# Optimization experiments

Measured on AMD Instinct MI355X. Metric: run time of the kernel, lower is better.

The kernel has to match this reference:

```python
import jax, jax.numpy as jnp
import numpy as np
from jax import lax

DN = ('NCH', 'OIH', 'NCH')

def conv1d(x, w, b, pad=0):
    y = lax.conv_general_dilated(x, w, window_strides=(1,), padding=[(pad, pad)], dimension_numbers=DN)
    return y + b[None, :, None]

def conv_transpose1d(x, w_torch, b):
    # torch ConvTranspose1d weight: [C_in, C_out, K]; equivalent to full conv with flipped kernel
    k = w_torch.shape[-1]
    w = jnp.flip(jnp.transpose(w_torch, (1, 0, 2)), axis=-1)  # [C_out, C_in, K]
    y = lax.conv_general_dilated(x, w, window_strides=(1,), padding=[(k - 1, k - 1)], dimension_numbers=DN)
    return y + b[None, :, None]

def converter(signal, w1, b1, w2, b2, wt, bt, w3, b3):
    h = jax.nn.relu(conv1d(signal, w1, b1))          # [B,10,n-2]
    h = jax.nn.relu(conv1d(h, w2, b2))               # [B,10,n-2]
    h = jax.nn.relu(conv_transpose1d(h, wt, bt))     # [B,10,n]
    h = jax.nn.sigmoid(conv1d(h, w3, b3))            # [B,2,n]
    return h

def setup_inputs() -> dict:
    key = jax.random.key(0)
    ks = jax.random.split(key, 12)
    B, C, n = 32, 128, 8192
    signal = jax.random.normal(ks[0], (B, C, n), dtype=jnp.float32)
    curr_diag = jax.random.uniform(ks[1], (B, n - 1), dtype=jnp.float32) + 0.5
    s = 0.1
    return {
        'signal': signal,
        'curr_diag': curr_diag,
        'index_diag': 1,
        'w1': jax.random.normal(ks[2], (10, C, 3), dtype=jnp.float32) * s,
        'b1': jax.random.normal(ks[3], (10,), dtype=jnp.float32) * s,
        'w2': jax.random.normal(ks[4], (10, 10, 1), dtype=jnp.float32) * s,
        'b2': jax.random.normal(ks[5], (10,), dtype=jnp.float32) * s,
        'wt': jax.random.normal(ks[6], (10, 10, 3), dtype=jnp.float32) * s,
        'bt': jax.random.normal(ks[7], (10,), dtype=jnp.float32) * s,
        'w3': jax.random.normal(ks[8], (2, 10, 1), dtype=jnp.float32) * s,
        'b3': jax.random.normal(ks[9], (2,), dtype=jnp.float32) * s,
        'const': jnp.float32(0.99),
    }

def reference(signal, curr_diag, index_diag, w1, b1, w2, b2, wt, bt, w3, b3, const):
    n = signal.shape[-1]
    lr = converter(signal, w1, b1, w2, b2, wt, bt, w3, b3)  # [B,2,n]
    left, right = lr[:, 0, :], lr[:, 1, :]
    # diag_len = n - index_diag; next diag has length diag_len - 1
    mass_in = curr_diag[:, 1:] * right[:, 1:n - index_diag]
    mass_in = mass_in + curr_diag[:, :-1] * left[:, index_diag:n - 1]
    mass_out = right[:, 0:n - index_diag - 1] + left[:, index_diag + 1:n]
    next_diag = const * mass_in / mass_out
    next_diag = jnp.log(next_diag)
    next_diag = next_diag - jnp.mean(next_diag)
    return next_diag
```

## Files before the change

kernel.cpp:

```cpp
#include <hip/hip_runtime.h>
#include <math.h>

#define B     32
#define CIN   128
#define NN    8192
#define N1    8190
#define CH    10
#define TOUT  252
#define NTILE 33

__global__ void k0_prep(const float* __restrict__ w1, float* __restrict__ wT)
{
    const int i = blockIdx.x * 256 + threadIdx.x;
    if (i < CIN * 32) {
        const int ci = i >> 5, r = i & 31;
        float v = 0.f;
        if (r < 30) {
            const int o = r / 3, k = r - o * 3;
            v = w1[(o * CIN + ci) * 3 + k];
        }
        wT[i] = v;
    }
}

__global__ __launch_bounds__(256, 4) void k_main(
    const float* __restrict__ sig, const float* __restrict__ wT,
    const float* __restrict__ b1, const float* __restrict__ w2, const float* __restrict__ b2,
    const float* __restrict__ wt, const float* __restrict__ bt,
    const float* __restrict__ w3, const float* __restrict__ b3,
    const float* __restrict__ cd, const float* __restrict__ cstp,
    float* __restrict__ outv, float* __restrict__ bsums)
{
    __shared__ float h2s[CH * 256];
    __shared__ float lsh[256], rsh[256];
    __shared__ float red[256];

    const int tid = threadIdx.x;
    const int b   = blockIdx.y;
    const int t0  = blockIdx.x * TOUT;
    const int g   = t0 - 2 + tid;
    const bool gvalid = (g >= 0) && (g < N1);
    const bool sh = (g > NN - 4);
    int gl = (g < 0) ? 0 : g;
    if (gl > NN - 4) gl = NN - 4;
    const float* sb = sig + (size_t)b * CIN * NN + gl;

    float y[CH];
#pragma unroll
    for (int o = 0; o < CH; ++o) y[o] = b1[o];

    for (int c = 0; c < 8; ++c) {
        float4 v[16];
#pragma unroll
        for (int j = 0; j < 16; ++j)
            v[j] = *(const float4*)(sb + (size_t)(c * 16 + j) * NN);

        const float* wbase = wT + c * 16 * 32;
#pragma unroll
        for (int j = 0; j < 16; ++j) {
            const float s0 = sh ? v[j].y : v[j].x;
            const float s1 = sh ? v[j].z : v[j].y;
            const float s2 = sh ? v[j].w : v[j].z;
            const float* wrow = wbase + j * 32;
#pragma unroll
            for (int o = 0; o < CH; ++o) {
                y[o] = fmaf(wrow[o * 3 + 0], s0, y[o]);
                y[o] = fmaf(wrow[o * 3 + 1], s1, y[o]);
                y[o] = fmaf(wrow[o * 3 + 2], s2, y[o]);
            }
        }
    }

#pragma unroll
    for (int o = 0; o < CH; ++o) y[o] = fmaxf(y[o], 0.f);
#pragma unroll
    for (int o = 0; o < CH; ++o) {
        float a = b2[o];
#pragma unroll
        for (int i = 0; i < CH; ++i) a = fmaf(w2[o * CH + i], y[i], a);
        h2s[o * 256 + tid] = gvalid ? fmaxf(a, 0.f) : 0.f;
    }
    __syncthreads();

    const int s = t0 + tid;
    if (tid < 254 && s < NN) {
        float acc[CH];
#pragma unroll
        for (int o = 0; o < CH; ++o) acc[o] = bt[o];
#pragma unroll
        for (int i = 0; i < CH; ++i) {
            const float a0 = h2s[i * 256 + tid];
            const float a1 = h2s[i * 256 + tid + 1];
            const float a2 = h2s[i * 256 + tid + 2];
            const float* wp = wt + i * CH * 3;
#pragma unroll
            for (int o = 0; o < CH; ++o) {
                acc[o] = fmaf(wp[o * 3 + 0], a2, acc[o]);
                acc[o] = fmaf(wp[o * 3 + 1], a1, acc[o]);
                acc[o] = fmaf(wp[o * 3 + 2], a0, acc[o]);
            }
        }
        float l = b3[0], r = b3[1];
#pragma unroll
        for (int o = 0; o < CH; ++o) {
            const float h3 = fmaxf(acc[o], 0.f);
            l = fmaf(w3[o],      h3, l);
            r = fmaf(w3[CH + o], h3, r);
        }
        lsh[tid] = 1.f / (1.f + __expf(-l));
        rsh[tid] = 1.f / (1.f + __expf(-r));
    }
    __syncthreads();

    float vlog = 0.f;
    const int t = t0 + tid;
    if (tid < TOUT && t < N1) {
        const float c0 = cd[(size_t)b * (NN - 1) + t];
        const float c1 = cd[(size_t)b * (NN - 1) + t + 1];
        const float mi = c1 * rsh[tid + 1] + c0 * lsh[tid + 1];
        const float mo = rsh[tid] + lsh[tid + 2];
        vlog = __logf(cstp[0] * mi / mo);
        outv[(size_t)b * N1 + t] = vlog;
    }

    red[tid] = vlog;
    __syncthreads();
#pragma unroll
    for (int st = 128; st > 0; st >>= 1) {
        if (tid < st) red[tid] += red[tid + st];
        __syncthreads();
    }
    if (tid == 0) bsums[blockIdx.y * NTILE + blockIdx.x] = red[0];
}

__global__ __launch_bounds__(256) void k3_meansub(
    const float* __restrict__ bsums, float* __restrict__ outv, int n)
{
    __shared__ float red[256];
    const int tid = threadIdx.x;
    float s = 0.f;
    for (int i = tid; i < NTILE * B; i += 256) s += bsums[i];
    red[tid] = s;
    __syncthreads();
#pragma unroll
    for (int st = 128; st > 0; st >>= 1) {
        if (tid < st) red[tid] += red[tid + st];
        __syncthreads();
    }
    const float mean = red[0] / (float)(B * N1);
    __syncthreads();
    const int i = blockIdx.x * 256 + tid;
    if (i < n) outv[i] -= mean;
}

extern "C" void kernel_launch(void* const* d_in, const int* in_sizes, int n_in,
                              void* d_out, int out_size, void* d_ws, size_t ws_size,
                              hipStream_t stream)
{
    const float* sig = (const float*)d_in[0];
    const float* cd  = (const float*)d_in[1];
    const float* w1  = (const float*)d_in[3];
    const float* b1  = (const float*)d_in[4];
    const float* w2  = (const float*)d_in[5];
    const float* b2  = (const float*)d_in[6];
    const float* wt  = (const float*)d_in[7];
    const float* bt  = (const float*)d_in[8];
    const float* w3  = (const float*)d_in[9];
    const float* b3  = (const float*)d_in[10];
    const float* cst = (const float*)d_in[11];

    float* outv = (float*)d_out;

    float* ws   = (float*)d_ws;
    float* wT   = ws;
    float* bsum = wT + CIN * 32;

    dim3 blk(256);

    k0_prep   <<<dim3(16), blk, 0, stream>>>(w1, wT);
    k_main    <<<dim3(NTILE, B), blk, 0, stream>>>(sig, wT, b1, w2, b2,
                                                   wt, bt, w3, b3, cd, cst, outv, bsum);
    k3_meansub<<<dim3((out_size + 255) / 256), blk, 0, stream>>>(bsum, outv, out_size);
}
```

Baseline: 243.8 us.

## Stage signal chunks into LDS via direct global-to-LDS loads

Replaces the per-thread float4 register loads of 16 channels with wave-cooperative global_load_lds transfers into a shared buffer. Each thread then reads its three-tap window from LDS. The output tile shrinks to 244 columns with 34 tiles, and the tile start is clamped so every load stays a full aligned 256-column row. The aim is fully coalesced aligned loads with lower register pressure. The cost is extra barriers per chunk, serialised load and compute with no double buffering, and more halo overlap between tiles.

```diff
diff --git a/kernel.cpp b/kernel.cpp
--- a/kernel.cpp
+++ b/kernel.cpp
@@ -1,13 +1,23 @@
 #include <hip/hip_runtime.h>
 #include <math.h>
 
-#define B     32
-#define CIN   128
-#define NN    8192
-#define N1    8190
-#define CH    10
-#define TOUT  252
-#define NTILE 33
+#define B      32
+#define CIN    128
+#define NN     8192
+#define N1     8190
+#define CH     10
+#define TOUT   244
+#define NTILE  34
+#define SCOLS  256
+#define CPC    16
+#define NCHUNK (CIN / CPC)
+
+__device__ __forceinline__ void load_lds16(const float* g, float* l)
+{
+    __builtin_amdgcn_global_load_lds(
+        (const __attribute__((address_space(1))) void*)g,
+        (__attribute__((address_space(3))) void*)l, 16, 0, 0);
+}
 
 __global__ void k0_prep(const float* __restrict__ w1, float* __restrict__ wT)
 {
@@ -31,46 +41,55 @@
     const float* __restrict__ cd, const float* __restrict__ cstp,
     float* __restrict__ outv, float* __restrict__ bsums)
 {
+    __shared__ float sigb[CPC * SCOLS];
     __shared__ float h2s[CH * 256];
-    __shared__ float lsh[256], rsh[256];
-    __shared__ float red[256];
-
-    const int tid = threadIdx.x;
-    const int b   = blockIdx.y;
-    const int t0  = blockIdx.x * TOUT;
-    const int g   = t0 - 2 + tid;
-    const bool gvalid = (g >= 0) && (g < N1);
-    const bool sh = (g > NN - 4);
-    int gl = (g < 0) ? 0 : g;
-    if (gl > NN - 4) gl = NN - 4;
-    const float* sb = sig + (size_t)b * CIN * NN + gl;
+    __shared__ float lsh[256], rsh[256], red[256];
+
+    const int tid  = threadIdx.x;
+    const int lane = tid & 63;
+    const int wv   = tid >> 6;
+    const int b    = blockIdx.y;
+    const int t0   = blockIdx.x * TOUT;
+
+    int s0 = t0 - 4;
+    if (s0 < 0) s0 = 0;
+    if (s0 > NN - SCOLS) s0 = NN - SCOLS;
+    const int d0 = t0 - s0;
+
+    const float* gb = sig + (size_t)b * CIN * NN + s0 + lane * 4;
+
+    const int tc = (tid < 254) ? tid : 253;
 
     float y[CH];
 #pragma unroll
     for (int o = 0; o < CH; ++o) y[o] = b1[o];
 
-    for (int c = 0; c < 8; ++c) {
-        float4 v[16];
-#pragma unroll
-        for (int j = 0; j < 16; ++j)
-            v[j] = *(const float4*)(sb + (size_t)(c * 16 + j) * NN);
-
-        const float* wbase = wT + c * 16 * 32;
-#pragma unroll
-        for (int j = 0; j < 16; ++j) {
-            const float s0 = sh ? v[j].y : v[j].x;
-            const float s1 = sh ? v[j].z : v[j].y;
-            const float s2 = sh ? v[j].w : v[j].z;
+    for (int c = 0; c < NCHUNK; ++c) {
+        if (c) __syncthreads();
+#pragma unroll
+        for (int r = 0; r < 4; ++r) {
+            const int ch = c * CPC + wv * 4 + r;
+            load_lds16(gb + (size_t)ch * NN, &sigb[(wv * 4 + r) * SCOLS]);
+        }
+        __syncthreads();
+
+        const float* wbase = wT + c * CPC * 32;
+#pragma unroll
+        for (int j = 0; j < CPC; ++j) {
+            const float v0 = sigb[j * SCOLS + tc];
+            const float v1 = sigb[j * SCOLS + tc + 1];
+            const float v2 = sigb[j * SCOLS + tc + 2];
             const float* wrow = wbase + j * 32;
 #pragma unroll
             for (int o = 0; o < CH; ++o) {
-                y[o] = fmaf(wrow[o * 3 + 0], s0, y[o]);
-                y[o] = fmaf(wrow[o * 3 + 1], s1, y[o]);
-                y[o] = fmaf(wrow[o * 3 + 2], s2, y[o]);
+                y[o] = fmaf(wrow[o * 3 + 0], v0, y[o]);
+                y[o] = fmaf(wrow[o * 3 + 1], v1, y[o]);
+                y[o] = fmaf(wrow[o * 3 + 2], v2, y[o]);
             }
         }
     }
 
+    const int g = s0 + tid;
 #pragma unroll
     for (int o = 0; o < CH; ++o) y[o] = fmaxf(y[o], 0.f);
 #pragma unroll
@@ -78,20 +97,21 @@
         float a = b2[o];
 #pragma unroll
         for (int i = 0; i < CH; ++i) a = fmaf(w2[o * CH + i], y[i], a);
-        h2s[o * 256 + tid] = gvalid ? fmaxf(a, 0.f) : 0.f;
+        h2s[o * 256 + tid] = (tid <= 253 && g < N1) ? fmaxf(a, 0.f) : 0.f;
     }
     __syncthreads();
 
     const int s = t0 + tid;
-    if (tid < 254 && s < NN) {
+    if (tid <= TOUT + 2 && s < NN) {
+        const int ib = tid + d0 - 2;
         float acc[CH];
 #pragma unroll
         for (int o = 0; o < CH; ++o) acc[o] = bt[o];
 #pragma unroll
         for (int i = 0; i < CH; ++i) {
-            const float a0 = h2s[i * 256 + tid];
-            const float a1 = h2s[i * 256 + tid + 1];
-            const float a2 = h2s[i * 256 + tid + 2];
+            const float a0 = (ib >= 0)     ? h2s[i * 256 + ib]     : 0.f;
+            const float a1 = (ib + 1 >= 0) ? h2s[i * 256 + ib + 1] : 0.f;
+            const float a2 =                 h2s[i * 256 + ib + 2];
             const float* wp = wt + i * CH * 3;
 #pragma unroll
             for (int o = 0; o < CH; ++o) {
```

After: 250.6 us. 1.03x slower.
